# Kernel optimization log

Measured on AMD Instinct MI355X. Metric: run time of the kernel, lower is better.

The kernel has to match this reference:

```python
import jax, jax.numpy as jnp
import numpy as np

B, C, H = 4, 512, 4096
IC = C // 2


def setup_inputs() -> dict:
    key = jax.random.key(0)
    ks = jax.random.split(key, 9)
    s = 0.02
    return {
        "x": jax.random.normal(ks[0], (B, C, H), dtype=jnp.float32),
        "w_phi": jax.random.normal(ks[1], (IC, C), dtype=jnp.float32) * s,
        "b_phi": jax.random.normal(ks[2], (IC,), dtype=jnp.float32) * s,
        "w_theta": jax.random.normal(ks[3], (IC, C), dtype=jnp.float32) * s,
        "b_theta": jax.random.normal(ks[4], (IC,), dtype=jnp.float32) * s,
        "w_g": jax.random.normal(ks[5], (IC, C), dtype=jnp.float32) * s,
        "b_g": jax.random.normal(ks[6], (IC,), dtype=jnp.float32) * s,
        "w_mask": jax.random.normal(ks[7], (C, IC), dtype=jnp.float32) * s,
        "b_mask": jax.random.normal(ks[8], (C,), dtype=jnp.float32) * s,
    }


def reference(x, w_phi, b_phi, w_theta, b_theta, w_g, b_g, w_mask, b_mask):
    # conv1d kernel_size=1 == channel matmul. x: [b, c, h]
    phi = jnp.einsum('ic,bch->bih', w_phi, x) + b_phi[None, :, None]      # [b, ic, h]
    theta = jnp.einsum('ic,bch->bhi', w_theta, x) + b_theta[None, None, :]  # [b, h, ic]
    g = jnp.einsum('ic,bch->bhi', w_g, x) + b_g[None, None, :]             # [b, h, ic]
    scores = jnp.einsum('bqi,bik->bqk', theta, phi)                        # [b, h, h]
    # torch Softmax(dim=1) on [b, h_q, h_k] normalizes over the QUERY axis (axis=1)
    attn = jax.nn.softmax(scores, axis=1)
    ag = jnp.einsum('bqk,bki->bqi', attn, g)                               # [b, h, ic]
    mask = jnp.einsum('ci,bhi->bch', w_mask, ag) + b_mask[None, :, None]   # [b, c, h]
    return mask + x
```

## Files before the change

kernel.cpp:

```cpp
#include <hip/hip_runtime.h>
#include <hip/hip_bf16.h>
#include <hip/hip_fp16.h>
#include <type_traits>

constexpr int BB = 4;
constexpr int CC = 512;
constexpr int HH = 4096;
constexpr int IC = 256;

typedef _Float16 f16x8v __attribute__((ext_vector_type(8)));
typedef __bf16   bf16x8v __attribute__((ext_vector_type(8)));
typedef float    f32x4v __attribute__((ext_vector_type(4)));

__device__ __forceinline__ void gll16(const void* g, void* l) {
  __builtin_amdgcn_global_load_lds(
      (const __attribute__((address_space(1))) unsigned int*)g,
      (__attribute__((address_space(3))) unsigned int*)l, 16, 0, 0);
}

__device__ __forceinline__ f32x4v mfma16(f16x8v a, f16x8v b, f32x4v c) {
  return __builtin_amdgcn_mfma_f32_16x16x32_f16(a, b, c, 0, 0, 0);
}
__device__ __forceinline__ f32x4v mfma16(bf16x8v a, bf16x8v b, f32x4v c) {
  return __builtin_amdgcn_mfma_f32_16x16x32_bf16(a, b, c, 0, 0, 0);
}

__device__ __forceinline__ unsigned short hbits(float f) {
  __half h = __float2half(f);
  unsigned short b; __builtin_memcpy(&b, &h, 2); return b;
}
__device__ __forceinline__ unsigned short bbits(float f) {
  __hip_bfloat16 h = __float2bfloat16(f);
  unsigned short b; __builtin_memcpy(&b, &h, 2); return b;
}

template <int MODE, int BK>
__launch_bounds__(256)
__global__ void mgemm128(const void* __restrict__ Aall, const void* __restrict__ Ball,
                         const void* __restrict__ Ball2,
                         void* __restrict__ outP, void* __restrict__ out2P,
                         const float* __restrict__ bias, const float* __restrict__ bias2,
                         const float* __restrict__ xres, float* __restrict__ Z,
                         int M, int N, int K,
                         size_t sAb, size_t sBb, size_t sOb) {
  constexpr int CPR = BK / 8;
  constexpr int XM = (BK >= 64) ? 7 : 0;

  __shared__ __align__(16) unsigned short sA[128 * BK];
  __shared__ __align__(16) unsigned short sB[128 * BK];

  const int zz = blockIdx.z;
  int b, which;
  if constexpr (MODE == 0) { b = zz & (BB - 1); which = zz >> 2; }
  else { b = zz; which = 0; }

  const unsigned short* __restrict__ A = (const unsigned short*)Aall + (size_t)b * sAb;
  const unsigned short* __restrict__ Bm =
      (const unsigned short*)((MODE == 0 && which) ? Ball2 : Ball) + (size_t)b * sBb;
  const float* __restrict__ biasSel = (MODE == 0 && which) ? bias2 : bias;
  void* __restrict__ outSel = (MODE == 0 && which) ? out2P : outP;

  const int t = threadIdx.x;
  const int lane = t & 63;
  const int w = t >> 6;
  const int wm = (w >> 1) << 6;
  const int wn = (w & 1) << 6;
  const int mBase = blockIdx.y * 128;
  const int nBase = blockIdx.x * 128;

  const int fr = lane & 15;
  const int fo = (lane >> 4) << 3;
  const int fc = fo >> 3;

  f32x4v acc[4][4] = {};

  for (int k0 = 0; k0 < K; k0 += BK) {
#pragma unroll
    for (int p = 0; p < CPR / 2; ++p) {
      const int u = t + (p << 8);
      const int r = u / CPR;
      const int c = u & (CPR - 1);
      const int cs = (c ^ (r & XM)) << 3;
      gll16(A + (size_t)(mBase + r) * K + (k0 + cs), sA + u * 8);
      if constexpr (MODE == 3) {
        const unsigned short* s0 = Bm + (size_t)(nBase + r) * K + (k0 + cs);
        const f16x8v v0 = *(const f16x8v*)s0;
        const f16x8v v1 = *(const f16x8v*)(s0 + (size_t)BB * HH * IC);
        *(f16x8v*)(sB + u * 8) = v0 + v1;
      } else {
        gll16(Bm + (size_t)(nBase + r) * K + (k0 + cs), sB + u * 8);
      }
    }
    __syncthreads();
#pragma unroll
    for (int ks = 0; ks < BK / 32; ++ks) {
      f16x8v af[4], bf[4];
#pragma unroll
      for (int i = 0; i < 4; ++i) {
        const int row = wm + (i << 4) + fr;
        const int phys = ((ks << 2) + fc) ^ (row & XM);
        af[i] = *(const f16x8v*)(sA + row * BK + (phys << 3));
      }
#pragma unroll
      for (int j = 0; j < 4; ++j) {
        const int row = wn + (j << 4) + fr;
        const int phys = ((ks << 2) + fc) ^ (row & XM);
        bf[j] = *(const f16x8v*)(sB + row * BK + (phys << 3));
      }
#pragma unroll
      for (int i = 0; i < 4; ++i)
#pragma unroll
        for (int j = 0; j < 4; ++j)
          acc[i][j] = mfma16(af[i], bf[j], acc[i][j]);
    }
    __syncthreads();
  }

  const int row0 = (lane >> 4) << 2;
  const int col = lane & 15;

  if constexpr (MODE == 2) {
    __hip_bfloat16* __restrict__ outB = (__hip_bfloat16*)outP;
    float csum[4] = {0.f, 0.f, 0.f, 0.f};
#pragma unroll
    for (int i = 0; i < 4; ++i) {
      const int m0 = mBase + wm + (i << 4) + row0;
#pragma unroll
      for (int j = 0; j < 4; ++j) {
        const int n = nBase + wn + (j << 4) + col;
        __hip_bfloat16* dst = outB + (size_t)b * sOb + (size_t)m0 * N + n;
#pragma unroll
        for (int rg = 0; rg < 4; ++rg) {
          const float e = __expf(acc[i][j][rg]);
          dst[(size_t)rg * N] = __float2bfloat16(e);
          csum[j] += e;
        }
      }
    }
#pragma unroll
    for (int j = 0; j < 4; ++j) {
      float s = csum[j];
      s += __shfl_xor(s, 16, 64);
      s += __shfl_xor(s, 32, 64);
      if (lane < 16) {
        const int n = nBase + wn + (j << 4) + col;
        atomicAdd(&Z[(size_t)b * N + n], s);
      }
    }
  } else {
    float rzv[4];
    if constexpr (MODE == 1) {
#pragma unroll
      for (int j = 0; j < 4; ++j) {
        const int n = nBase + wn + (j << 4) + col;
        rzv[j] = 1.0f / Z[(size_t)b * N + n];
      }
    }
#pragma unroll
    for (int i = 0; i < 4; ++i) {
      const int m0 = mBase + wm + (i << 4) + row0;
#pragma unroll
      for (int j = 0; j < 4; ++j) {
        const int n = nBase + wn + (j << 4) + col;
#pragma unroll
        for (int rg = 0; rg < 4; ++rg) {
          const int m = m0 + rg;
          const float v = acc[i][j][rg];
          if constexpr (MODE == 0) {
            ((__half*)outSel)[(size_t)b * sOb + (size_t)m * N + n] =
                __float2half(v + biasSel[n]);
          } else if constexpr (MODE == 1) {
            ((__hip_bfloat16*)outP)[(size_t)b * sOb + (size_t)m * N + n] =
                __float2bfloat16((v + bias[m]) * rzv[j]);
          } else {
            const size_t o = (size_t)b * sOb + (size_t)m * N + n;
            ((float*)outP)[o] = v + bias[m] + xres[o];
          }
        }
      }
    }
  }
  (void)M;
}

__launch_bounds__(256)
__global__ void mgemm_ag(const __hip_bfloat16* __restrict__ Gall,
                         const __hip_bfloat16* __restrict__ Eall,
                         unsigned short* __restrict__ P16) {
  constexpr int KC = 2048;
  constexpr int BK = 128;
  __shared__ __align__(16) unsigned short sG[256 * BK];
  __shared__ __align__(16) unsigned short sE[64 * BK];

  const int b = blockIdx.z;
  const int kc = blockIdx.x;
  const int qBase = blockIdx.y * 64;
  const int k0base = kc * KC;

  const unsigned short* __restrict__ G =
      (const unsigned short*)Gall + (size_t)b * IC * HH;
  const unsigned short* __restrict__ E =
      (const unsigned short*)Eall + (size_t)b * HH * HH;

  const int t = threadIdx.x;
  const int lane = t & 63;
  const int w = t >> 6;
  const int fr = lane & 15;
  const int fo = (lane >> 4) << 3;
  const int fc = fo >> 3;

  f32x4v acc[4][4] = {};

  for (int kk = 0; kk < KC; kk += BK) {
    const int k0 = k0base + kk;
#pragma unroll
    for (int p = 0; p < 4; ++p) {
      const int u = t + (p << 8);
      const int row = u >> 4;
      const int csrc = (u & 15) ^ (row & 7);
      gll16(E + (size_t)(qBase + row) * HH + k0 + (csrc << 3), sE + u * 8);
    }
#pragma unroll
    for (int p = 0; p < 16; ++p) {
      const int u = t + (p << 8);
      const int row = u >> 4;
      const int csrc = (u & 15) ^ (row & 7);
      gll16(G + (size_t)row * HH + k0 + (csrc << 3), sG + u * 8);
    }
    __syncthreads();
#pragma unroll
    for (int ks = 0; ks < 4; ++ks) {
      bf16x8v af[4], bfv[4];
      const int c16 = (ks << 2) + fc;
#pragma unroll
      for (int i = 0; i < 4; ++i) {
        const int row = (w << 6) + (i << 4) + fr;
        af[i] = *(const bf16x8v*)(sG + row * BK + ((c16 ^ (row & 7)) << 3));
      }
#pragma unroll
      for (int j = 0; j < 4; ++j) {
        const int row = (j << 4) + fr;
        bfv[j] = *(const bf16x8v*)(sE + row * BK + ((c16 ^ (row & 7)) << 3));
      }
#pragma unroll
      for (int i = 0; i < 4; ++i)
#pragma unroll
        for (int j = 0; j < 4; ++j)
          acc[i][j] = mfma16(af[i], bfv[j], acc[i][j]);
    }
    __syncthreads();
  }

  unsigned short* __restrict__ P =
      P16 + ((size_t)kc * BB + b) * HH * IC;
  const int quad = lane >> 4;
  const int col = lane & 15;
#pragma unroll
  for (int i = 0; i < 4; ++i) {
    const int ic0 = (w << 6) + (i << 4) + (quad << 2);
#pragma unroll
    for (int j = 0; j < 4; ++j) {
      const int q = qBase + (j << 4) + col;
      ushort4 s = {hbits(acc[i][j][0]), hbits(acc[i][j][1]),
                   hbits(acc[i][j][2]), hbits(acc[i][j][3])};
      *(ushort4*)(P + (size_t)q * IC + ic0) = s;
    }
  }
}

__launch_bounds__(256)
__global__ void xpose(const float* __restrict__ x, __half* __restrict__ xT,
                      const float* __restrict__ w0, const float* __restrict__ w1,
                      const float* __restrict__ w2, const float* __restrict__ w3,
                      __half* __restrict__ d0, __half* __restrict__ d1,
                      __half* __restrict__ d2, __half* __restrict__ d3) {
  if (blockIdx.y == CC / 64) {
    const int which = blockIdx.z;
    const float* s = which == 0 ? w0 : (which == 1 ? w1 : (which == 2 ? w2 : w3));
    __half* d = which == 0 ? d0 : (which == 1 ? d1 : (which == 2 ? d2 : d3));
    const int i = ((int)blockIdx.x * 256 + (int)threadIdx.x) * 8;
    const float4 v0 = *(const float4*)(s + i);
    const float4 v1 = *(const float4*)(s + i + 4);
    __half h[8] = {__float2half(v0.x), __float2half(v0.y), __float2half(v0.z),
                   __float2half(v0.w), __float2half(v1.x), __float2half(v1.y),
                   __float2half(v1.z), __float2half(v1.w)};
    uint4 pack; __builtin_memcpy(&pack, h, 16);
    *(uint4*)(d + i) = pack;
    return;
  }
  __shared__ float tile[64][65];
  const int b = blockIdx.z;
  const int h0 = blockIdx.x * 64;
  const int c0 = blockIdx.y * 64;
  const int lane = threadIdx.x & 63;
  const int r0 = threadIdx.x >> 6;
  const float* xb = x + (size_t)b * CC * HH;
#pragma unroll
  for (int rr = 0; rr < 16; ++rr) {
    const int c = r0 * 16 + rr;
    tile[c][lane] = xb[(size_t)(c0 + c) * HH + h0 + lane];
  }
  __syncthreads();
  __half* ob = xT + (size_t)b * HH * CC;
#pragma unroll
  for (int rr = 0; rr < 16; ++rr) {
    const int hl = r0 * 16 + rr;
    ob[(size_t)(h0 + hl) * CC + c0 + lane] = __float2half(tile[lane][hl]);
  }
}

extern "C" void kernel_launch(void* const* d_in, const int* in_sizes, int n_in,
                              void* d_out, int out_size, void* d_ws, size_t ws_size,
                              hipStream_t stream) {
  (void)in_sizes; (void)n_in; (void)out_size; (void)ws_size;

  const float* x       = (const float*)d_in[0];
  const float* w_phi   = (const float*)d_in[1];
  const float* b_phi   = (const float*)d_in[2];
  const float* w_theta = (const float*)d_in[3];
  const float* b_theta = (const float*)d_in[4];
  const float* w_g     = (const float*)d_in[5];
  const float* b_g     = (const float*)d_in[6];
  const float* w_mask  = (const float*)d_in[7];
  const float* b_mask  = (const float*)d_in[8];
  float* out = (float*)d_out;

  char* p = (char*)d_ws;
  __hip_bfloat16* E = (__hip_bfloat16*)p;           p += (size_t)BB * HH * HH * 2;
  __half* xT       = (__half*)p;                    p += (size_t)BB * HH * CC * 2;
  __half* thetaH   = (__half*)p;                    p += (size_t)BB * HH * IC * 2;
  __half* phiH     = (__half*)p;                    p += (size_t)BB * HH * IC * 2;
  __hip_bfloat16* gB  = (__hip_bfloat16*)p;         p += (size_t)BB * IC * HH * 2;
  __half* wthH = (__half*)p;                        p += (size_t)IC * CC * 2;
  __half* wphH = (__half*)p;                        p += (size_t)IC * CC * 2;
  __half* wgH  = (__half*)p;                        p += (size_t)IC * CC * 2;
  __half* wmH  = (__half*)p;                        p += (size_t)CC * IC * 2;
  float* Z = (float*)p;                             p += (size_t)BB * HH * 4;
  unsigned short* P16 = (unsigned short*)xT;

  const dim3 blk(256);

  xpose<<<dim3(HH / 64, CC / 64 + 1, BB), blk, 0, stream>>>(
      x, xT, w_phi, w_theta, w_g, w_mask, wphH, wthH, wgH, wmH);

  hipMemsetAsync(Z, 0, (size_t)BB * HH * sizeof(float), stream);

  mgemm128<0, 64><<<dim3(IC / 128, HH / 128, BB * 2), blk, 0, stream>>>(
      xT, wthH, wphH, thetaH, phiH, b_theta, b_phi, nullptr, nullptr,
      HH, IC, CC, (size_t)HH * CC, 0, (size_t)HH * IC);

  mgemm128<2, 64><<<dim3(HH / 128, HH / 128, BB), blk, 0, stream>>>(
      thetaH, phiH, nullptr, E, nullptr, nullptr, nullptr, nullptr, Z,
      HH, HH, IC, (size_t)HH * IC, (size_t)HH * IC, (size_t)HH * HH);

  mgemm128<1, 64><<<dim3(HH / 128, IC / 128, BB), blk, 0, stream>>>(
      wgH, xT, nullptr, gB, nullptr, b_g, nullptr, nullptr, Z,
      IC, HH, CC, 0, (size_t)HH * CC, (size_t)IC * HH);

  mgemm_ag<<<dim3(2, HH / 64, BB), blk, 0, stream>>>(gB, E, P16);

  mgemm128<3, 64><<<dim3(HH / 128, CC / 128, BB), blk, 0, stream>>>(
      wmH, P16, nullptr, out, nullptr, b_mask, nullptr, x, nullptr,
      CC, HH, IC, 0, (size_t)HH * IC, (size_t)CC * HH);
}
```

Before: 253.6 us.

## Double-buffer LDS tiles in attention-times-G GEMM to overlap loads with MFMA

Splits the K tile in mgemm_ag from 128 to 64 and allocates two LDS buffers for G and E. The global-to-LDS loads for the next tile are issued before the MFMA work on the current tile, so memory latency can hide behind compute. This costs twice as many barriers per K range and smaller per-stage MFMA batches. Total LDS use stays the same.

```diff
diff --git a/kernel.cpp b/kernel.cpp
--- a/kernel.cpp
+++ b/kernel.cpp
@@ -188,9 +188,9 @@
                          const __hip_bfloat16* __restrict__ Eall,
                          unsigned short* __restrict__ P16) {
   constexpr int KC = 2048;
-  constexpr int BK = 128;
-  __shared__ __align__(16) unsigned short sG[256 * BK];
-  __shared__ __align__(16) unsigned short sE[64 * BK];
+  constexpr int BK = 64;
+  __shared__ __align__(16) unsigned short sG[2][256 * BK];
+  __shared__ __align__(16) unsigned short sE[2][64 * BK];
 
   const int b = blockIdx.z;
   const int kc = blockIdx.x;
@@ -211,36 +211,38 @@
 
   f32x4v acc[4][4] = {};
 
-  for (int kk = 0; kk < KC; kk += BK) {
-    const int k0 = k0base + kk;
-#pragma unroll
-    for (int p = 0; p < 4; ++p) {
+  auto stage = [&](unsigned short* dG, unsigned short* dE, int k0) {
+#pragma unroll
+    for (int p = 0; p < 2; ++p) {
       const int u = t + (p << 8);
-      const int row = u >> 4;
-      const int csrc = (u & 15) ^ (row & 7);
-      gll16(E + (size_t)(qBase + row) * HH + k0 + (csrc << 3), sE + u * 8);
-    }
-#pragma unroll
-    for (int p = 0; p < 16; ++p) {
+      const int row = u >> 3;
+      const int c = u & 7;
+      gll16(E + (size_t)(qBase + row) * HH + k0 + ((c ^ (row & 7)) << 3),
+            dE + u * 8);
+    }
+#pragma unroll
+    for (int p = 0; p < 8; ++p) {
       const int u = t + (p << 8);
-      const int row = u >> 4;
-      const int csrc = (u & 15) ^ (row & 7);
-      gll16(G + (size_t)row * HH + k0 + (csrc << 3), sG + u * 8);
-    }
-    __syncthreads();
-#pragma unroll
-    for (int ks = 0; ks < 4; ++ks) {
+      const int row = u >> 3;
+      const int c = u & 7;
+      gll16(G + (size_t)row * HH + k0 + ((c ^ (row & 7)) << 3), dG + u * 8);
+    }
+  };
+
+  auto compute = [&](const unsigned short* pG, const unsigned short* pE) {
+#pragma unroll
+    for (int ks = 0; ks < 2; ++ks) {
       bf16x8v af[4], bfv[4];
       const int c16 = (ks << 2) + fc;
 #pragma unroll
       for (int i = 0; i < 4; ++i) {
         const int row = (w << 6) + (i << 4) + fr;
-        af[i] = *(const bf16x8v*)(sG + row * BK + ((c16 ^ (row & 7)) << 3));
+        af[i] = *(const bf16x8v*)(pG + row * BK + ((c16 ^ (row & 7)) << 3));
       }
 #pragma unroll
       for (int j = 0; j < 4; ++j) {
         const int row = (j << 4) + fr;
-        bfv[j] = *(const bf16x8v*)(sE + row * BK + ((c16 ^ (row & 7)) << 3));
+        bfv[j] = *(const bf16x8v*)(pE + row * BK + ((c16 ^ (row & 7)) << 3));
       }
 #pragma unroll
       for (int i = 0; i < 4; ++i)
@@ -248,6 +250,17 @@
         for (int j = 0; j < 4; ++j)
           acc[i][j] = mfma16(af[i], bfv[j], acc[i][j]);
     }
+  };
+
+  stage(sG[0], sE[0], k0base);
+  __syncthreads();
+  for (int kk = 0; kk < KC; kk += 2 * BK) {
+    stage(sG[1], sE[1], k0base + kk + BK);
+    compute(sG[0], sE[0]);
+    __syncthreads();
+    if (kk + 2 * BK < KC)
+      stage(sG[0], sE[0], k0base + kk + 2 * BK);
+    compute(sG[1], sE[1]);
     __syncthreads();
   }
 
```

After: 250.5 us (median of 2 runs). Within noise of the previous version (-1.2%).
